# Kernel optimization log

Hardware: AMD Instinct MI355X
Metric: run time of the kernel (lower is better)

## Reference

```python
import jax, jax.numpy as jnp
import numpy as np

B, IMG_DIM, H, W = 2, 256, 64, 64
PC_C, PC_D = 16, 16          # voxel_dim = PC_C * PC_D = 256
VOXEL_DIM = PC_C * PC_D
QK_DIM = 256                 # out_channels of img_conv / voxel_conv


def _conv1x1(x, w, b):
    # x: [B, Cin, H, W], w: [Cout, Cin], b: [Cout]  (1x1 conv == per-pixel matmul)
    return jnp.einsum('bchw,oc->bohw', x, w) + b[None, :, None, None]


def setup_inputs() -> dict:
    key = jax.random.key(0)
    ks = jax.random.split(key, 10)
    s = 0.02
    return {
        'img': jax.random.normal(ks[0], (B, IMG_DIM, H, W), jnp.float32),
        'pc': jax.random.normal(ks[1], (B, PC_D, H, W, PC_C), jnp.float32),  # dense() layout [B,D,H,W,C]
        'img_conv_w': jax.random.normal(ks[2], (QK_DIM, IMG_DIM), jnp.float32) * s,
        'img_conv_b': jnp.zeros((QK_DIM,), jnp.float32),
        'voxel_conv_w': jax.random.normal(ks[3], (QK_DIM, VOXEL_DIM), jnp.float32) * s,
        'voxel_conv_b': jnp.zeros((QK_DIM,), jnp.float32),
        'img_v_w': jax.random.normal(ks[4], (IMG_DIM, IMG_DIM), jnp.float32) * s,
        'img_v_b': jnp.zeros((IMG_DIM,), jnp.float32),
        'voxel_v_w': jax.random.normal(ks[5], (VOXEL_DIM, VOXEL_DIM), jnp.float32) * s,
        'voxel_v_b': jnp.zeros((VOXEL_DIM,), jnp.float32),
    }


def reference(img, pc, img_conv_w, img_conv_b, voxel_conv_w, voxel_conv_b,
              img_v_w, img_v_b, voxel_v_w, voxel_v_b):
    b, c_img, h, w = img.shape
    # pc.dense() -> permute(0,4,1,2,3) -> [B, C, D, H, W] -> [B, C*D, H, W]
    pc = jnp.transpose(pc, (0, 4, 1, 2, 3))
    pcb, pcc, pcd, pch, pcw = pc.shape
    pc2 = pc.reshape(pcb, pcc * pcd, pch, pcw)
    n = h * w  # == pch * pcw (required by the bmms)

    img_q = _conv1x1(img, img_conv_w, img_conv_b).reshape(b, QK_DIM, n).transpose(0, 2, 1)  # [B, N, 256]
    pc_k = _conv1x1(pc2, voxel_conv_w, voxel_conv_b).reshape(b, QK_DIM, n)                  # [B, 256, N]
    # unscaled single-head cross attention, softmax over voxel positions
    attn = jax.nn.softmax(jnp.einsum('bnc,bcm->bnm', img_q, pc_k), axis=-1)                 # [B, N_img, N_pc]

    img_v = _conv1x1(img, img_v_w, img_v_b).reshape(b, c_img, n)                            # [B, C_img, N]
    img_v = jnp.einsum('bcn,bmn->bcm', img_v, attn).reshape(b, c_img, h, w)                 # img_v @ attn^T

    pc_v = _conv1x1(pc2, voxel_v_w, voxel_v_b).reshape(b, pcc * pcd, n)                     # [B, C*D, N]
    pc_v = jnp.einsum('bcn,bmn->bcm', pc_v, attn).reshape(b, pcc, pcd, pch, pcw)
    return (img_v, pc_v)
```

## Files before the change

kernel.cpp:

```cpp
#include <hip/hip_runtime.h>
#include <hip/hip_bf16.h>


typedef __hip_bfloat16 bf16;
typedef __attribute__((ext_vector_type(8))) short bf16x8;
typedef __attribute__((ext_vector_type(4))) float f32x4;

#define AS1 __attribute__((address_space(1)))
#define AS3 __attribute__((address_space(3)))

__device__ __forceinline__ void gld_lds16(const bf16* g, bf16* s) {
    __builtin_amdgcn_global_load_lds((const AS1 void*)g, (AS3 void*)s, 16, 0, 0);
}

__device__ __forceinline__ bf16x8 cvt8(const float* __restrict__ p) {
    const float4 a = *(const float4*)p;
    const float4 b = *(const float4*)(p + 4);
    bf16 t[8];
    t[0] = __float2bfloat16(a.x); t[1] = __float2bfloat16(a.y);
    t[2] = __float2bfloat16(a.z); t[3] = __float2bfloat16(a.w);
    t[4] = __float2bfloat16(b.x); t[5] = __float2bfloat16(b.y);
    t[6] = __float2bfloat16(b.z); t[7] = __float2bfloat16(b.w);
    return *(const bf16x8*)t;
}

__global__ __launch_bounds__(256) void proj_kernel(
    const float* __restrict__ img, const float* __restrict__ pc,
    const float* __restrict__ Wq,  const float* __restrict__ bq,
    const float* __restrict__ Wk,  const float* __restrict__ bk,
    const float* __restrict__ Wvi, const float* __restrict__ bvi,
    const float* __restrict__ Wvp, const float* __restrict__ bvp,
    bf16* __restrict__ Qw, bf16* __restrict__ Ktw, bf16* __restrict__ Vall)
{
    __shared__ __align__(16) bf16 XT[64][264];

    const int blk = blockIdx.x;
    const int s   = blk >> 8;
    const int b   = (blk >> 7) & 1;
    const int g   = (blk >> 6) & 1;
    const int n0  = (blk & 63) * 64;
    const int tid = threadIdx.x;

    if (s == 0) {
        const float* src = img + b * 1048576;
        for (int k = 0; k < 16; k++) {
            const int i = tid + k * 256;
            const int cin = i >> 4, nl4 = (i & 15) * 4;
            const float4 v = *(const float4*)&src[cin * 4096 + n0 + nl4];
            XT[nl4 + 0][cin] = __float2bfloat16(v.x);
            XT[nl4 + 1][cin] = __float2bfloat16(v.y);
            XT[nl4 + 2][cin] = __float2bfloat16(v.z);
            XT[nl4 + 3][cin] = __float2bfloat16(v.w);
        }
    } else {
        const float* src = pc + b * 1048576;
        for (int k = 0; k < 16; k++) {
            const int d = k, u = tid;
            const int nl = u >> 2, c4 = (u & 3) * 4;
            const float4 v = *(const float4*)&src[d * 65536 + (n0 + nl) * 16 + c4];
            XT[nl][(c4 + 0) * 16 + d] = __float2bfloat16(v.x);
            XT[nl][(c4 + 1) * 16 + d] = __float2bfloat16(v.y);
            XT[nl][(c4 + 2) * 16 + d] = __float2bfloat16(v.z);
            XT[nl][(c4 + 3) * 16 + d] = __float2bfloat16(v.w);
        }
    }
    __syncthreads();

    const float* W = s ? (g ? Wvp : Wk) : (g ? Wvi : Wq);
    const float* Bv = s ? (g ? bvp : bk) : (g ? bvi : bq);

    const int wv = tid >> 6, lane = tid & 63, l16 = lane & 15, quad = lane >> 4;
    const int ob = wv * 64;

    f32x4 acc[4][4] = {};

    for (int ks = 0; ks < 8; ks++) {
        const int k0 = ks * 32;
        bf16x8 af[4], wf[4];
        for (int ti = 0; ti < 4; ti++)
            af[ti] = *(const bf16x8*)&XT[ti * 16 + l16][k0 + quad * 8];
        for (int tj = 0; tj < 4; tj++)
            wf[tj] = cvt8(&W[(ob + tj * 16 + l16) * 256 + k0 + quad * 8]);
        for (int ti = 0; ti < 4; ti++)
            for (int tj = 0; tj < 4; tj++)
                acc[ti][tj] = __builtin_amdgcn_mfma_f32_16x16x32_bf16(af[ti], wf[tj], acc[ti][tj], 0, 0, 0);
    }

    if (g == 0) {
        bf16* D1 = (s ? Ktw : Qw) + b * (4096 * 256);
        for (int tj = 0; tj < 4; tj++) {
            const int o = ob + tj * 16 + l16;
            const float bias = Bv[o];
            for (int ti = 0; ti < 4; ti++) {
                const int nl = ti * 16 + quad * 4;
                for (int r = 0; r < 4; r++)
                    D1[(n0 + nl + r) * 256 + o] = __float2bfloat16(acc[ti][tj][r] + bias);
            }
        }
    } else {
        bf16* D2 = Vall + b * (512 * 4096) + (s ? 256 * 4096 : 0);
        for (int tj = 0; tj < 4; tj++) {
            const int o = ob + tj * 16 + l16;
            const float bias = Bv[o];
            for (int ti = 0; ti < 4; ti++) {
                const int nl = ti * 16 + quad * 4;
                bf16 pv[4];
                for (int r = 0; r < 4; r++)
                    pv[r] = __float2bfloat16(acc[ti][tj][r] + bias);
                *(uint2*)&D2[o * 4096 + n0 + nl] = *(const uint2*)pv;
            }
        }
    }
}

__global__ __launch_bounds__(256, 4) void attn_s_kernel(
    const bf16* __restrict__ Qw, const bf16* __restrict__ Ktw,
    bf16* __restrict__ Pt, float* __restrict__ Lpart)
{
    __shared__ __align__(16) bf16 smem[2][8192];

    const int b  = blockIdx.z;
    const int q0 = blockIdx.y * 128;
    const int p0 = blockIdx.x * 128;
    const bf16* Aq = Qw  + b * (4096 * 256);
    const bf16* Ak = Ktw + b * (4096 * 256);

    const int tid = threadIdx.x;
    const int wv = tid >> 6, lane = tid & 63, l16 = lane & 15, quad = lane >> 4;
    const int wr = wv >> 1, wc = wv & 1;

    int aoff[4], boff[4];
    for (int t = 0; t < 4; t++) {
        const int rowa = wr * 64 + t * 16 + l16;
        aoff[t] = rowa * 32 + (quad ^ ((rowa >> 1) & 3)) * 8;
        const int rowb = wc * 64 + t * 16 + l16;
        boff[t] = rowb * 32 + (quad ^ ((rowb >> 1) & 3)) * 8;
    }

    const int arow0 = tid >> 2;
    const int kswz = ((tid & 3) ^ ((arow0 >> 1) & 3)) * 8;
    const bf16* Ag0 = Ak + (p0 + arow0) * 256 + kswz;
    const bf16* Ag1 = Ak + (p0 + 64 + arow0) * 256 + kswz;
    const bf16* Bg0 = Aq + (q0 + arow0) * 256 + kswz;
    const bf16* Bg1 = Aq + (q0 + 64 + arow0) * 256 + kswz;

    f32x4 acc[4][4] = {};

#define SSTAGE(buf, ks)                                                 \
    do {                                                                \
        const int _k = (ks) * 32;                                       \
        bf16* _s = &smem[(buf)][0];                                     \
        gld_lds16(Ag0 + _k, _s + tid * 8);                              \
        gld_lds16(Ag1 + _k, _s + 2048 + tid * 8);                       \
        gld_lds16(Bg0 + _k, _s + 4096 + tid * 8);                       \
        gld_lds16(Bg1 + _k, _s + 6144 + tid * 8);                       \
    } while (0)

    SSTAGE(0, 0);
    int cur = 0;
    for (int ks = 0; ks < 8; ks++) {
        if (ks + 1 < 8) {
            SSTAGE(cur ^ 1, ks + 1);
            asm volatile("s_waitcnt vmcnt(4)" ::: "memory");
        } else {
            asm volatile("s_waitcnt vmcnt(0)" ::: "memory");
        }
        __builtin_amdgcn_s_barrier();
        __builtin_amdgcn_sched_barrier(0);

        const bf16* As_ = &smem[cur][0];
        const bf16* Bs_ = &smem[cur][4096];
        bf16x8 af[4], bfr[4];
        for (int t = 0; t < 4; t++) af[t]  = *(const bf16x8*)&As_[aoff[t]];
        for (int t = 0; t < 4; t++) bfr[t] = *(const bf16x8*)&Bs_[boff[t]];
        __builtin_amdgcn_s_setprio(1);
        for (int ti = 0; ti < 4; ti++)
            for (int tj = 0; tj < 4; tj++)
                acc[ti][tj] = __builtin_amdgcn_mfma_f32_16x16x32_bf16(af[ti], bfr[tj], acc[ti][tj], 0, 0, 0);
        __builtin_amdgcn_s_setprio(0);

        asm volatile("s_waitcnt lgkmcnt(0)" ::: "memory");
        __builtin_amdgcn_s_barrier();
        cur ^= 1;
    }
#undef SSTAGE

    bf16* Pdst = Pt + (size_t)b * 4096 * 4096;
    const int strip = blockIdx.x * 2 + wr;
    for (int tj = 0; tj < 4; tj++) {
        const int q = q0 + wc * 64 + tj * 16 + l16;
        float partial = 0.0f;
        for (int ti = 0; ti < 4; ti++) {
            const int p = p0 + wr * 64 + ti * 16 + quad * 4;
            bf16 pv[4];
            for (int r = 0; r < 4; r++) {
                const float e = __expf(fminf(acc[ti][tj][r], 80.0f));
                partial += e;
                pv[r] = __float2bfloat16(e);
            }
            *(uint2*)&Pdst[(size_t)q * 4096 + p] = *(const uint2*)pv;
        }
        partial += __shfl_xor(partial, 16);
        partial += __shfl_xor(partial, 32);
        if (lane < 16)
            Lpart[(size_t)(b * 4096 + q) * 64 + strip] = partial;
    }
}

__global__ __launch_bounds__(256) void lred_kernel(
    const float* __restrict__ Lpart, float* __restrict__ Linv)
{
    const int row = blockIdx.x * 256 + threadIdx.x;
    const float4* lp = (const float4*)&Lpart[(size_t)row * 64];
    float s = 0.0f;
    for (int i = 0; i < 16; i++) {
        const float4 v = lp[i];
        s += v.x + v.y + v.z + v.w;
    }
    Linv[row] = 1.0f / fmaxf(s, 1e-30f);
}

__global__ __launch_bounds__(512, 4) void attn_o_kernel(
    const bf16* __restrict__ Vall, const bf16* __restrict__ Pt,
    const float* __restrict__ Linv, float* __restrict__ out)
{
    __shared__ __align__(16) bf16 smem[2][2][6144];

    const int b  = blockIdx.z;
    const int c0 = blockIdx.y * 128;
    const int q0 = blockIdx.x * 64;
    const bf16* A = Vall + (size_t)b * 512 * 4096;
    const bf16* B = Pt   + (size_t)b * 4096 * 4096;

    const int tid = threadIdx.x;
    const int grp = tid >> 8;
    const int t8  = tid & 255;
    const int wv = t8 >> 6, lane = t8 & 63, l16 = lane & 15, quad = lane >> 4;
    const int wr = wv >> 1, wc = wv & 1;

    int aoff[4], boff[2];
    for (int t = 0; t < 4; t++) {
        const int row = wr * 64 + t * 16 + l16;
        aoff[t] = row * 32 + (quad ^ ((row >> 1) & 3)) * 8;
    }
    for (int t = 0; t < 2; t++) {
        const int row = wc * 32 + t * 16 + l16;
        boff[t] = row * 32 + (quad ^ ((row >> 1) & 3)) * 8;
    }

    const int arow = t8 >> 2;
    const int kswz = ((t8 & 3) ^ ((arow >> 1) & 3)) * 8;
    const bf16* Ag0 = A + (c0 + arow) * 4096 + grp * 2048 + kswz;
    const bf16* Ag1 = A + (c0 + 64 + arow) * 4096 + grp * 2048 + kswz;
    const bf16* Bg  = B + (q0 + arow) * 4096 + grp * 2048 + kswz;

    f32x4 acc[4][2] = {};

#define STAGE(buf, ks)                                                  \
    do {                                                                \
        const int _k = (ks) * 32;                                       \
        bf16* _s = &smem[grp][(buf)][0];                                \
        gld_lds16(Ag0 + _k, _s + t8 * 8);                               \
        gld_lds16(Ag1 + _k, _s + 2048 + t8 * 8);                        \
        gld_lds16(Bg  + _k, _s + 4096 + t8 * 8);                        \
    } while (0)

    STAGE(0, 0);
    int cur = 0;
    for (int ks = 0; ks < 64; ks++) {
        if (ks + 1 < 64) {
            STAGE(cur ^ 1, ks + 1);
            asm volatile("s_waitcnt vmcnt(3)" ::: "memory");
        } else {
            asm volatile("s_waitcnt vmcnt(0)" ::: "memory");
        }
        __builtin_amdgcn_s_barrier();
        __builtin_amdgcn_sched_barrier(0);

        const bf16* As_ = &smem[grp][cur][0];
        const bf16* Bs_ = &smem[grp][cur][4096];
        bf16x8 af[4], bfr[2];
        for (int t = 0; t < 4; t++) af[t]  = *(const bf16x8*)&As_[aoff[t]];
        for (int t = 0; t < 2; t++) bfr[t] = *(const bf16x8*)&Bs_[boff[t]];
        __builtin_amdgcn_s_setprio(1);
        for (int ti = 0; ti < 4; ti++)
            for (int tj = 0; tj < 2; tj++)
                acc[ti][tj] = __builtin_amdgcn_mfma_f32_16x16x32_bf16(af[ti], bfr[tj], acc[ti][tj], 0, 0, 0);
        __builtin_amdgcn_s_setprio(0);

        asm volatile("s_waitcnt lgkmcnt(0)" ::: "memory");
        __builtin_amdgcn_s_barrier();
        cur ^= 1;
    }
#undef STAGE

    __syncthreads();

    float* comb = (float*)&smem[0][0];
    const int sl0 = (wr * 64 + quad * 4) * 64 + wc * 32 + l16;
    if (grp == 0) {
        for (int ti = 0; ti < 4; ti++)
            for (int tj = 0; tj < 2; tj++)
                for (int r = 0; r < 4; r++)
                    comb[sl0 + (ti * 16 + r) * 64 + tj * 16] = acc[ti][tj][r];
    }
    __syncthreads();
    if (grp == 1) {
        for (int ti = 0; ti < 4; ti++)
            for (int tj = 0; tj < 2; tj++)
                for (int r = 0; r < 4; r++)
                    comb[sl0 + (ti * 16 + r) * 64 + tj * 16] += acc[ti][tj][r];
    }
    __syncthreads();

    const int f0 = tid * 16;
    const int cl = f0 >> 6, ql = f0 & 63;
    const int c_ = c0 + cl;
    const size_t base = (c_ < 256)
        ? ((size_t)b * 1048576 + (size_t)c_ * 4096)
        : (2097152u + (size_t)b * 1048576 + (size_t)(c_ - 256) * 4096);
    for (int j = 0; j < 4; j++) {
        const float4 v = *(const float4*)&comb[f0 + j * 4];
        const float4 l = *(const float4*)&Linv[b * 4096 + q0 + ql + j * 4];
        float4 o;
        o.x = v.x * l.x; o.y = v.y * l.y; o.z = v.z * l.z; o.w = v.w * l.w;
        *(float4*)&out[base + q0 + ql + j * 4] = o;
    }
}

extern "C" void kernel_launch(void* const* d_in, const int* in_sizes, int n_in,
                              void* d_out, int out_size, void* d_ws, size_t ws_size,
                              hipStream_t stream)
{
    const float* img = (const float*)d_in[0];
    const float* pc  = (const float*)d_in[1];
    const float* Wq  = (const float*)d_in[2];
    const float* bq  = (const float*)d_in[3];
    const float* Wk  = (const float*)d_in[4];
    const float* bk  = (const float*)d_in[5];
    const float* Wvi = (const float*)d_in[6];
    const float* bvi = (const float*)d_in[7];
    const float* Wvp = (const float*)d_in[8];
    const float* bvp = (const float*)d_in[9];

    char* ws = (char*)d_ws;
    bf16*  Qw    = (bf16*)(ws);
    bf16*  Ktw   = (bf16*)(ws + (4ull  << 20));
    bf16*  Vall  = (bf16*)(ws + (8ull  << 20));
    bf16*  Pt    = (bf16*)(ws + (16ull << 20));
    float* Lpart = (float*)(ws + (80ull << 20));
    float* Linv  = (float*)(ws + (82ull << 20));

    proj_kernel<<<512, 256, 0, stream>>>(img, pc, Wq, bq, Wk, bk,
                                         Wvi, bvi, Wvp, bvp, Qw, Ktw, Vall);
    attn_s_kernel<<<dim3(32, 32, 2), 256, 0, stream>>>(Qw, Ktw, Pt, Lpart);
    lred_kernel<<<32, 256, 0, stream>>>(Lpart, Linv);
    attn_o_kernel<<<dim3(64, 4, 2), 512, 0, stream>>>(Vall, Pt, Linv, (float*)d_out);
}
```

Measured before the change: 199.4 us.

## Enlarge attn_o tile to 128x128 and remap blocks for XCD-aware scheduling

After: 192.6 us. 1.04x faster.

```diff
diff --git a/kernel.cpp b/kernel.cpp
--- a/kernel.cpp
+++ b/kernel.cpp
@@ -220,15 +220,19 @@
     Linv[row] = 1.0f / fmaxf(s, 1e-30f);
 }
 
-__global__ __launch_bounds__(512, 4) void attn_o_kernel(
+__global__ __launch_bounds__(512, 2) void attn_o_kernel(
     const bf16* __restrict__ Vall, const bf16* __restrict__ Pt,
     const float* __restrict__ Linv, float* __restrict__ out)
 {
-    __shared__ __align__(16) bf16 smem[2][2][6144];
-
-    const int b  = blockIdx.z;
-    const int c0 = blockIdx.y * 128;
-    const int q0 = blockIdx.x * 64;
+    __shared__ __align__(16) bf16 smem[2][2][8192];
+
+    const int orig = blockIdx.x;
+    const int L = (orig & 7) * 32 + (orig >> 3);
+    const int b   = L >> 7;
+    const int rem = L & 127;
+    const int c0  = (rem & 3) * 128;
+    const int q0  = (rem >> 2) * 128;
+
     const bf16* A = Vall + (size_t)b * 512 * 4096;
     const bf16* B = Pt   + (size_t)b * 4096 * 4096;
 
@@ -238,23 +242,23 @@
     const int wv = t8 >> 6, lane = t8 & 63, l16 = lane & 15, quad = lane >> 4;
     const int wr = wv >> 1, wc = wv & 1;
 
-    int aoff[4], boff[2];
+    int aoff[4], boff[4];
     for (int t = 0; t < 4; t++) {
-        const int row = wr * 64 + t * 16 + l16;
-        aoff[t] = row * 32 + (quad ^ ((row >> 1) & 3)) * 8;
-    }
-    for (int t = 0; t < 2; t++) {
-        const int row = wc * 32 + t * 16 + l16;
-        boff[t] = row * 32 + (quad ^ ((row >> 1) & 3)) * 8;
+        const int rowa = wr * 64 + t * 16 + l16;
+        aoff[t] = rowa * 32 + (quad ^ ((rowa >> 1) & 3)) * 8;
+        const int rowb = wc * 64 + t * 16 + l16;
+        boff[t] = rowb * 32 + (quad ^ ((rowb >> 1) & 3)) * 8;
     }
 
     const int arow = t8 >> 2;
     const int kswz = ((t8 & 3) ^ ((arow >> 1) & 3)) * 8;
-    const bf16* Ag0 = A + (c0 + arow) * 4096 + grp * 2048 + kswz;
-    const bf16* Ag1 = A + (c0 + 64 + arow) * 4096 + grp * 2048 + kswz;
-    const bf16* Bg  = B + (q0 + arow) * 4096 + grp * 2048 + kswz;
-
-    f32x4 acc[4][2] = {};
+    const int kb = grp * 2048 + kswz;
+    const bf16* Ag0 = A + (c0 + arow) * 4096 + kb;
+    const bf16* Ag1 = A + (c0 + 64 + arow) * 4096 + kb;
+    const bf16* Bg0 = B + (size_t)(q0 + arow) * 4096 + kb;
+    const bf16* Bg1 = B + (size_t)(q0 + 64 + arow) * 4096 + kb;
+
+    f32x4 acc[4][4] = {};
 
 #define STAGE(buf, ks)                                                  \
     do {                                                                \
@@ -262,7 +266,8 @@
         bf16* _s = &smem[grp][(buf)][0];                                \
         gld_lds16(Ag0 + _k, _s + t8 * 8);                               \
         gld_lds16(Ag1 + _k, _s + 2048 + t8 * 8);                        \
-        gld_lds16(Bg  + _k, _s + 4096 + t8 * 8);                        \
+        gld_lds16(Bg0 + _k, _s + 4096 + t8 * 8);                        \
+        gld_lds16(Bg1 + _k, _s + 6144 + t8 * 8);                        \
     } while (0)
 
     STAGE(0, 0);
@@ -270,7 +275,7 @@
     for (int ks = 0; ks < 64; ks++) {
         if (ks + 1 < 64) {
             STAGE(cur ^ 1, ks + 1);
-            asm volatile("s_waitcnt vmcnt(3)" ::: "memory");
+            asm volatile("s_waitcnt vmcnt(4)" ::: "memory");
         } else {
             asm volatile("s_waitcnt vmcnt(0)" ::: "memory");
         }
@@ -279,12 +284,12 @@
 
         const bf16* As_ = &smem[grp][cur][0];
         const bf16* Bs_ = &smem[grp][cur][4096];
-        bf16x8 af[4], bfr[2];
+        bf16x8 af[4], bfr[4];
         for (int t = 0; t < 4; t++) af[t]  = *(const bf16x8*)&As_[aoff[t]];
-        for (int t = 0; t < 2; t++) bfr[t] = *(const bf16x8*)&Bs_[boff[t]];
+        for (int t = 0; t < 4; t++) bfr[t] = *(const bf16x8*)&Bs_[boff[t]];
         __builtin_amdgcn_s_setprio(1);
         for (int ti = 0; ti < 4; ti++)
-            for (int tj = 0; tj < 2; tj++)
+            for (int tj = 0; tj < 4; tj++)
                 acc[ti][tj] = __builtin_amdgcn_mfma_f32_16x16x32_bf16(af[ti], bfr[tj], acc[ti][tj], 0, 0, 0);
         __builtin_amdgcn_s_setprio(0);
 
@@ -296,35 +301,35 @@
 
     __syncthreads();
 
-    float* comb = (float*)&smem[0][0];
-    const int sl0 = (wr * 64 + quad * 4) * 64 + wc * 32 + l16;
+    float* comb = (float*)&smem[0][0][0];
     if (grp == 0) {
         for (int ti = 0; ti < 4; ti++)
-            for (int tj = 0; tj < 2; tj++)
+            for (int tj = 0; tj < 4; tj++)
                 for (int r = 0; r < 4; r++)
-                    comb[sl0 + (ti * 16 + r) * 64 + tj * 16] = acc[ti][tj][r];
+                    comb[(wr * 64 + ti * 16 + quad * 4 + r) * 128 + wc * 64 + tj * 16 + l16]
+                        = acc[ti][tj][r];
     }
     __syncthreads();
     if (grp == 1) {
         for (int ti = 0; ti < 4; ti++)
-            for (int tj = 0; tj < 2; tj++)
+            for (int tj = 0; tj < 4; tj++)
                 for (int r = 0; r < 4; r++)
-                    comb[sl0 + (ti * 16 + r) * 64 + tj * 16] += acc[ti][tj][r];
+                    comb[(wr * 64 + ti * 16 + quad * 4 + r) * 128 + wc * 64 + tj * 16 + l16]
+                        += acc[ti][tj][r];
     }
     __syncthreads();
 
-    const int f0 = tid * 16;
-    const int cl = f0 >> 6, ql = f0 & 63;
+    const int cl = tid >> 2, qb = (tid & 3) * 32;
     const int c_ = c0 + cl;
     const size_t base = (c_ < 256)
         ? ((size_t)b * 1048576 + (size_t)c_ * 4096)
         : (2097152u + (size_t)b * 1048576 + (size_t)(c_ - 256) * 4096);
-    for (int j = 0; j < 4; j++) {
-        const float4 v = *(const float4*)&comb[f0 + j * 4];
-        const float4 l = *(const float4*)&Linv[b * 4096 + q0 + ql + j * 4];
+    for (int j = 0; j < 8; j++) {
+        const float4 v = *(const float4*)&comb[cl * 128 + qb + j * 4];
+        const float4 l = *(const float4*)&Linv[b * 4096 + q0 + qb + j * 4];
         float4 o;
         o.x = v.x * l.x; o.y = v.y * l.y; o.z = v.z * l.z; o.w = v.w * l.w;
-        *(float4*)&out[base + q0 + ql + j * 4] = o;
+        *(float4*)&out[base + q0 + qb + j * 4] = o;
     }
 }
 
@@ -355,5 +360,5 @@
                                          Wvi, bvi, Wvp, bvp, Qw, Ktw, Vall);
     attn_s_kernel<<<dim3(32, 32, 2), 256, 0, stream>>>(Qw, Ktw, Pt, Lpart);
     lred_kernel<<<32, 256, 0, stream>>>(Lpart, Linv);
-    attn_o_kernel<<<dim3(64, 4, 2), 512, 0, stream>>>(Vall, Pt, Linv, (float*)d_out);
-}
+    attn_o_kernel<<<256, 512, 0, stream>>>(Vall, Pt, Linv, (float*)d_out);
+}
```
